# Kernel optimization log

Hardware: AMD Instinct MI355X
Metric: run time of the kernel (lower is better)

Reference implementation:

```python
import jax, jax.numpy as jnp
import numpy as np

N_TOKEN = 267735
D_PROJ = 1024
CUTOFF_ENDS = [0, 20000, 40000, 200000, 267735]
D_EMBS = [1024, 256, 64, 16]  # d_embed // div_val**i, div_val=4
EMB_SCALE = float(D_PROJ) ** 0.5


def setup_inputs() -> dict:
    key = jax.random.key(0)
    ks = jax.random.split(key, 9)
    inp = jax.random.randint(ks[0], (8, 2048), 0, N_TOKEN)
    d = {"inp": inp}
    for i in range(4):
        size = CUTOFF_ENDS[i + 1] - CUTOFF_ENDS[i]
        de = D_EMBS[i]
        d[f"emb{i}"] = jax.random.normal(ks[1 + 2 * i], (size, de), jnp.float32) * 0.02
        d[f"proj{i}"] = jax.random.normal(ks[2 + 2 * i], (D_PROJ, de), jnp.float32) * 0.02
    return d


def reference(inp, emb0, emb1, emb2, emb3, proj0, proj1, proj2, proj3):
    embs = [emb0, emb1, emb2, emb3]
    projs = [proj0, proj1, proj2, proj3]
    flat = inp.reshape(-1)  # [T]
    out = jnp.zeros((flat.shape[0], D_PROJ), jnp.float32)
    for i in range(4):
        l, r = CUTOFF_ENDS[i], CUTOFF_ENDS[i + 1]
        mask = (flat >= l) & (flat < r)  # clusters are disjoint
        idx = jnp.clip(flat - l, 0, r - l - 1)  # in-range dummy where masked out
        # gather [T, d_emb_i] then project to [T, d_proj] (F.linear with weight [d_proj, d_emb_i])
        e = jnp.einsum('td,pd->tp', embs[i][idx], projs[i])
        out = jnp.where(mask[:, None], e, out)
    return (out * EMB_SCALE).reshape(*inp.shape, D_PROJ)
```

## Files before the change

### kernel.cpp

```cpp
#include <hip/hip_runtime.h>


#define CUT0 20000
#define CUT1 40000
#define CUT2 200000

#define PB1 (1024 * 1024)
#define PB2 (PB1 + 1024 * 256)
#define PB3 (PB2 + 1024 * 64)
#define PBEND (PB3 + 1024 * 32)

typedef __attribute__((ext_vector_type(8))) short bf16x8;
typedef __attribute__((ext_vector_type(8))) unsigned short u16x8;
typedef __attribute__((ext_vector_type(4))) float f32x4;

__device__ __forceinline__ unsigned short f2bf(float f) {
    unsigned u = __float_as_uint(f);
    u += 0x7FFFu + ((u >> 16) & 1u);
    return (unsigned short)(u >> 16);
}

__device__ __forceinline__ u16x8 cvt8(const float* __restrict__ s) {
    float4 a = *(const float4*)s;
    float4 b = *(const float4*)(s + 4);
    return (u16x8){f2bf(a.x), f2bf(a.y), f2bf(a.z), f2bf(a.w),
                   f2bf(b.x), f2bf(b.y), f2bf(b.z), f2bf(b.w)};
}

__device__ __forceinline__ void gl_lds16(const unsigned short* g, unsigned short* s) {
    __builtin_amdgcn_global_load_lds(
        (const __attribute__((address_space(1))) void*)g,
        (__attribute__((address_space(3))) void*)s, 16, 0, 0);
}

__global__ __launch_bounds__(256)
void classify_convert(const int* __restrict__ inp, unsigned* __restrict__ counters,
                      unsigned* __restrict__ lists, int T,
                      const float* __restrict__ proj0, const float* __restrict__ proj1,
                      const float* __restrict__ proj2, const float* __restrict__ proj3,
                      unsigned short* __restrict__ projbf) {
    int t = blockIdx.x * 256 + threadIdx.x;
    int lane = threadIdx.x & 63;
    bool valid = (t < T);
    int id = valid ? inp[t] : 0;
    int c = -1, l = 0;
    if (valid) {
        if (id < CUT0)      { c = 0; l = 0; }
        else if (id < CUT1) { c = 1; l = CUT0; }
        else if (id < CUT2) { c = 2; l = CUT1; }
        else                { c = 3; l = CUT2; }
    }
    #pragma unroll
    for (int i = 0; i < 4; ++i) {
        unsigned long long m = __ballot(c == i);
        if (c == i) {
            int leader = __ffsll(m) - 1;
            unsigned base = 0;
            if (lane == leader) base = atomicAdd(&counters[i], (unsigned)__popcll(m));
            base = __shfl(base, leader);
            unsigned rank = (unsigned)__popcll(m & ((1ull << lane) - 1ull));
            lists[(size_t)i * T + base + rank] = ((unsigned)t << 18) | (unsigned)(id - l);
        }
    }
    const int stride = gridDim.x * 256;
    for (int u = t; u < PBEND / 8; u += stride) {
        int base = u * 8;
        u16x8 o;
        if (base < PB1)       o = cvt8(proj0 + base);
        else if (base < PB2)  o = cvt8(proj1 + (base - PB1));
        else if (base < PB3)  o = cvt8(proj2 + (base - PB2));
        else {
            int rel = base - PB3;
            int row = rel >> 5, col = rel & 31;
            if (col < 16) o = cvt8(proj3 + row * 16 + col);
            else          o = (u16x8){0, 0, 0, 0, 0, 0, 0, 0};
        }
        *(u16x8*)(projbf + base) = o;
    }
}

__global__ __launch_bounds__(256)
void gather_bf16(const float* __restrict__ emb0, const float* __restrict__ emb1,
                 const unsigned* __restrict__ lists, const unsigned* __restrict__ counters,
                 int T, unsigned short* __restrict__ ecomp) {
    const int c0 = (int)counters[0], c1 = (int)counters[1];
    const size_t off1 = (size_t)((c0 + 63) & ~63) * 1024;
    const int n0 = c0 << 7, n1 = c1 << 5;
    const int total = n0 + n1;
    const int stride = gridDim.x * 256;
    for (int u = blockIdx.x * 256 + threadIdx.x; u < total; u += stride) {
        int v = u;
        if (v < n0) {
            int r = v >> 7, j = v & 127;
            unsigned id = lists[r] & 0x3FFFFu;
            *(u16x8*)(ecomp + (size_t)r * 1024 + j * 8) = cvt8(emb0 + (size_t)id * 1024 + j * 8);
        } else {
            v -= n0;
            int r = v >> 5, j = v & 31;
            unsigned id = lists[T + r] & 0x3FFFFu;
            *(u16x8*)(ecomp + off1 + (size_t)r * 256 + j * 8) = cvt8(emb1 + (size_t)id * 256 + j * 8);
        }
    }
}

template<int EK, int PK>
__device__ __forceinline__
void tile_shallow(const float* __restrict__ Ef, const unsigned short* __restrict__ P,
                  const unsigned* __restrict__ list, int count, int mtile, int ntile,
                  float* __restrict__ out) {
    constexpr int KST = PK / 32;
    const int m0 = mtile * 64;
    const int rows = min(64, count - m0);
    const int py = ntile * 128;
    const int tid = (int)threadIdx.x;
    const int lane = tid & 63;
    const int w  = tid >> 6;
    const int ln = lane & 15;
    const int qd = lane >> 4;

    const int arow = w * 16 + ln;
    const unsigned aid = (arow < rows) ? (list[m0 + arow] & 0x3FFFFu) : 0u;
    const float* ea = Ef + (size_t)aid * EK;
    const unsigned short* pb = P + (size_t)(py + ln) * PK + qd * 8;

    f32x4 acc[8];
    #pragma unroll
    for (int ct = 0; ct < 8; ++ct) acc[ct] = (f32x4){0.f, 0.f, 0.f, 0.f};

    #pragma unroll
    for (int s = 0; s < KST; ++s) {
        const int k = s * 32 + qd * 8;
        u16x8 av;
        if (k + 8 <= EK) av = cvt8(ea + k);
        else             av = (u16x8){0, 0, 0, 0, 0, 0, 0, 0};
        bf16x8 a = *(const bf16x8*)&av;
        #pragma unroll
        for (int ct = 0; ct < 8; ++ct) {
            bf16x8 b = *(const bf16x8*)(pb + (size_t)ct * 16 * PK + s * 32);
            acc[ct] = __builtin_amdgcn_mfma_f32_16x16x32_bf16(a, b, acc[ct], 0, 0, 0);
        }
    }

    int trow[4];
    #pragma unroll
    for (int r = 0; r < 4; ++r) {
        int row = w * 16 + qd * 4 + r;
        trow[r] = (row < rows) ? (int)(list[m0 + row] >> 18) : -1;
    }
    #pragma unroll
    for (int ct = 0; ct < 8; ++ct)
        #pragma unroll
        for (int r = 0; r < 4; ++r)
            if (trow[r] >= 0)
                out[(size_t)trow[r] * 1024 + py + ct * 16 + ln] = acc[ct][r] * 32.0f;
}

__global__ __launch_bounds__(256)
void gemm_shallow(const float* __restrict__ emb2, const float* __restrict__ emb3,
                  const unsigned short* __restrict__ projbf,
                  const unsigned* __restrict__ lists, const unsigned* __restrict__ counters,
                  int T, float* __restrict__ out) {
    const int c2 = (int)counters[2], c3 = (int)counters[3];
    const int g2 = (c2 + 63) >> 6;
    const int gt = g2 + ((c3 + 63) >> 6);

    const int xcd = blockIdx.x & 7;
    const int slot = blockIdx.x >> 3;
    const int nslots = gridDim.x >> 3;

    for (int i = slot; ; i += nslots) {
        const int g = ((i >> 3) << 3) + xcd;
        if (g >= gt) break;
        const int nt = i & 7;
        if (g < g2) tile_shallow<64, 64>(emb2, projbf + PB2, lists + 2 * T, c2, g,      nt, out);
        else        tile_shallow<16, 32>(emb3, projbf + PB3, lists + 3 * T, c3, g - g2, nt, out);
    }
}

template<int KP>
__device__ __forceinline__
void tile_gemm_lds(const unsigned short* __restrict__ E, const unsigned short* __restrict__ P,
                   const unsigned* __restrict__ list, int count, int mtile, int ntile,
                   float* __restrict__ out,
                   unsigned short* E_s, unsigned short* P_s, unsigned* pk_s) {
    constexpr int NCH = KP / 64;
    const int m0 = mtile * 64;
    const int rows = min(64, count - m0);
    const int py = ntile * 128;
    const int tid = (int)threadIdx.x;
    const int lane = tid & 63;
    const int w  = tid >> 6;
    const int ln = lane & 15;
    const int qd = lane >> 4;

    if (tid < 64) pk_s[tid] = (tid < rows) ? list[m0 + tid] : 0u;

    const unsigned short* eb = E + (size_t)m0 * KP;
    const unsigned short* pg = P + (size_t)py * KP;

    auto STAGE = [&](int h, int ch) {
        const int k0 = ch * 64;
        #pragma unroll
        for (int it = 0; it < 2; ++it) {
            int i16 = it * 256 + tid;
            int row = i16 >> 3, cc = (i16 & 7) ^ (row & 7);
            gl_lds16(eb + (size_t)row * KP + k0 + cc * 8, E_s + h * (64 * 64) + i16 * 8);
        }
        #pragma unroll
        for (int it = 0; it < 4; ++it) {
            int i16 = it * 256 + tid;
            int row = i16 >> 3, cc = (i16 & 7) ^ (row & 7);
            gl_lds16(pg + (size_t)row * KP + k0 + cc * 8, P_s + h * (128 * 64) + i16 * 8);
        }
    };

    f32x4 acc[8];
    #pragma unroll
    for (int ct = 0; ct < 8; ++ct) acc[ct] = (f32x4){0.f, 0.f, 0.f, 0.f};

    STAGE(0, 0);
    __syncthreads();
    int cur = 0;
    for (int ch = 0; ch < NCH; ++ch) {
        if (ch + 1 < NCH) STAGE(cur ^ 1, ch + 1);
        const unsigned short* Eb = E_s + cur * (64 * 64);
        const unsigned short* Pb = P_s + cur * (128 * 64);
        const int ar = w * 16 + ln;
        #pragma unroll
        for (int s = 0; s < 2; ++s) {
            bf16x8 a = *(const bf16x8*)(Eb + ar * 64 + (((s * 4 + qd) ^ (ar & 7)) * 8));
            #pragma unroll
            for (int ct = 0; ct < 8; ++ct) {
                const int br = ct * 16 + ln;
                bf16x8 b = *(const bf16x8*)(Pb + br * 64 + (((s * 4 + qd) ^ (br & 7)) * 8));
                acc[ct] = __builtin_amdgcn_mfma_f32_16x16x32_bf16(a, b, acc[ct], 0, 0, 0);
            }
        }
        __syncthreads();
        cur ^= 1;
    }

    #pragma unroll
    for (int ct = 0; ct < 8; ++ct) {
        #pragma unroll
        for (int r = 0; r < 4; ++r) {
            int row = w * 16 + qd * 4 + r;
            if (row < rows) {
                int t = (int)(pk_s[row] >> 18);
                out[(size_t)t * 1024 + py + ct * 16 + ln] = acc[ct][r] * 32.0f;
            }
        }
    }
    __syncthreads();
}

__global__ __launch_bounds__(256)
void gemm_deep(const unsigned short* __restrict__ ecomp, const unsigned short* __restrict__ projbf,
               const unsigned* __restrict__ lists, const unsigned* __restrict__ counters,
               int T, float* __restrict__ out) {
    __shared__ unsigned short E_s[2 * 64 * 64];
    __shared__ unsigned short P_s[2 * 128 * 64];
    __shared__ unsigned pk_s[64];

    const int c0 = (int)counters[0], c1 = (int)counters[1];
    const size_t off1 = (size_t)((c0 + 63) & ~63) * 1024;
    const int g0 = (c0 + 63) >> 6;
    const int gt = g0 + ((c1 + 63) >> 6);

    const int xcd = blockIdx.x & 7;
    const int slot = blockIdx.x >> 3;
    const int nslots = gridDim.x >> 3;

    for (int i = slot; ; i += nslots) {
        const int g = ((i >> 3) << 3) + xcd;
        if (g >= gt) break;
        const int nt = i & 7;
        if (g < g0) tile_gemm_lds<1024>(ecomp,        projbf,       lists,     c0, g,      nt, out, E_s, P_s, pk_s);
        else        tile_gemm_lds< 256>(ecomp + off1, projbf + PB1, lists + T, c1, g - g0, nt, out, E_s, P_s, pk_s);
    }
}

extern "C" void kernel_launch(void* const* d_in, const int* in_sizes, int n_in,
                              void* d_out, int out_size, void* d_ws, size_t ws_size,
                              hipStream_t stream) {
    const int*   inp   = (const int*)d_in[0];
    const float* emb0  = (const float*)d_in[1];
    const float* proj0 = (const float*)d_in[2];
    const float* emb1  = (const float*)d_in[3];
    const float* proj1 = (const float*)d_in[4];
    const float* emb2  = (const float*)d_in[5];
    const float* proj2 = (const float*)d_in[6];
    const float* emb3  = (const float*)d_in[7];
    const float* proj3 = (const float*)d_in[8];
    float* out = (float*)d_out;
    const int T = in_sizes[0];

    unsigned* counters = (unsigned*)d_ws;
    unsigned* lists    = (unsigned*)((char*)d_ws + 256);
    size_t lists_b = ((size_t)4 * T * 4 + 255) & ~(size_t)255;
    unsigned short* projbf = (unsigned short*)((char*)d_ws + 256 + lists_b);
    unsigned short* ecomp  = projbf + PBEND;

    hipMemsetAsync(counters, 0, 16, stream);
    classify_convert<<<dim3(512), 256, 0, stream>>>(inp, counters, lists, T,
                                                    proj0, proj1, proj2, proj3, projbf);
    gather_bf16<<<dim3(768), 256, 0, stream>>>(emb0, emb1, lists, counters, T, ecomp);
    gemm_shallow<<<dim3(2048), 256, 0, stream>>>(emb2, emb3, projbf, lists, counters, T, out);
    gemm_deep<<<dim3(768), 256, 0, stream>>>(ecomp, projbf, lists, counters, T, out);
}
```

Measured before the change: 226.2 us.

## Fuse embedding gather into deep GEMM and merge all cluster GEMMs into one kernel

Removes the separate gather_bf16 pass: deep tiles now read fp32 embedding rows directly by token id, convert to bf16 in registers, and write them into swizzled LDS. The shallow and deep GEMM kernels are merged into a single persistent launch covering all four clusters. The LDS double buffer becomes a single buffer, cutting shared memory and allowing an occupancy hint of 4 blocks per CU. This avoids the bf16 staging round-trip through global memory and two launches. In exchange, each of the 8 N-tiles per row tile re-gathers and re-converts the fp32 embeddings, and loads are no longer overlapped with MFMA.

New measurement: 222.1 us. No clear change (-1.8%).

```diff
diff --git a/kernel.cpp b/kernel.cpp
--- a/kernel.cpp
+++ b/kernel.cpp
@@ -79,29 +79,6 @@
     }
 }
 
-__global__ __launch_bounds__(256)
-void gather_bf16(const float* __restrict__ emb0, const float* __restrict__ emb1,
-                 const unsigned* __restrict__ lists, const unsigned* __restrict__ counters,
-                 int T, unsigned short* __restrict__ ecomp) {
-    const int c0 = (int)counters[0], c1 = (int)counters[1];
-    const size_t off1 = (size_t)((c0 + 63) & ~63) * 1024;
-    const int n0 = c0 << 7, n1 = c1 << 5;
-    const int total = n0 + n1;
-    const int stride = gridDim.x * 256;
-    for (int u = blockIdx.x * 256 + threadIdx.x; u < total; u += stride) {
-        int v = u;
-        if (v < n0) {
-            int r = v >> 7, j = v & 127;
-            unsigned id = lists[r] & 0x3FFFFu;
-            *(u16x8*)(ecomp + (size_t)r * 1024 + j * 8) = cvt8(emb0 + (size_t)id * 1024 + j * 8);
-        } else {
-            v -= n0;
-            int r = v >> 5, j = v & 31;
-            unsigned id = lists[T + r] & 0x3FFFFu;
-            *(u16x8*)(ecomp + off1 + (size_t)r * 256 + j * 8) = cvt8(emb1 + (size_t)id * 256 + j * 8);
-        }
-    }
-}
 
 template<int EK, int PK>
 __device__ __forceinline__
@@ -155,35 +132,13 @@
                 out[(size_t)trow[r] * 1024 + py + ct * 16 + ln] = acc[ct][r] * 32.0f;
 }
 
-__global__ __launch_bounds__(256)
-void gemm_shallow(const float* __restrict__ emb2, const float* __restrict__ emb3,
-                  const unsigned short* __restrict__ projbf,
-                  const unsigned* __restrict__ lists, const unsigned* __restrict__ counters,
-                  int T, float* __restrict__ out) {
-    const int c2 = (int)counters[2], c3 = (int)counters[3];
-    const int g2 = (c2 + 63) >> 6;
-    const int gt = g2 + ((c3 + 63) >> 6);
-
-    const int xcd = blockIdx.x & 7;
-    const int slot = blockIdx.x >> 3;
-    const int nslots = gridDim.x >> 3;
-
-    for (int i = slot; ; i += nslots) {
-        const int g = ((i >> 3) << 3) + xcd;
-        if (g >= gt) break;
-        const int nt = i & 7;
-        if (g < g2) tile_shallow<64, 64>(emb2, projbf + PB2, lists + 2 * T, c2, g,      nt, out);
-        else        tile_shallow<16, 32>(emb3, projbf + PB3, lists + 3 * T, c3, g - g2, nt, out);
-    }
-}
-
-template<int KP>
+template<int EK>
 __device__ __forceinline__
-void tile_gemm_lds(const unsigned short* __restrict__ E, const unsigned short* __restrict__ P,
-                   const unsigned* __restrict__ list, int count, int mtile, int ntile,
-                   float* __restrict__ out,
-                   unsigned short* E_s, unsigned short* P_s, unsigned* pk_s) {
-    constexpr int NCH = KP / 64;
+void tile_deep(const float* __restrict__ Ef, const unsigned short* __restrict__ P,
+               const unsigned* __restrict__ list, int count, int mtile, int ntile,
+               float* __restrict__ out,
+               unsigned short* E_s, unsigned short* P_s, unsigned* pk_s) {
+    constexpr int NCH = EK / 64;
     const int m0 = mtile * 64;
     const int rows = min(64, count - m0);
     const int py = ntile * 128;
@@ -195,49 +150,45 @@
 
     if (tid < 64) pk_s[tid] = (tid < rows) ? list[m0 + tid] : 0u;
 
-    const unsigned short* eb = E + (size_t)m0 * KP;
-    const unsigned short* pg = P + (size_t)py * KP;
-
-    auto STAGE = [&](int h, int ch) {
+    const int srow = tid >> 2;
+    const int sq4  = tid & 3;
+    const unsigned sid = (srow < rows) ? (list[m0 + srow] & 0x3FFFFu) : 0u;
+    const float* erow = Ef + (size_t)sid * EK + sq4 * 16;
+    const unsigned short* pg = P + (size_t)py * EK;
+
+    f32x4 acc[8];
+    #pragma unroll
+    for (int ct = 0; ct < 8; ++ct) acc[ct] = (f32x4){0.f, 0.f, 0.f, 0.f};
+
+    for (int ch = 0; ch < NCH; ++ch) {
         const int k0 = ch * 64;
-        #pragma unroll
-        for (int it = 0; it < 2; ++it) {
-            int i16 = it * 256 + tid;
-            int row = i16 >> 3, cc = (i16 & 7) ^ (row & 7);
-            gl_lds16(eb + (size_t)row * KP + k0 + cc * 8, E_s + h * (64 * 64) + i16 * 8);
+        {
+            u16x8 h0 = cvt8(erow + k0);
+            u16x8 h1 = cvt8(erow + k0 + 8);
+            const int ci = sq4 * 2;
+            *(u16x8*)&E_s[srow * 64 + ((ci       ^ (srow & 7)) * 8)] = h0;
+            *(u16x8*)&E_s[srow * 64 + (((ci + 1) ^ (srow & 7)) * 8)] = h1;
         }
         #pragma unroll
         for (int it = 0; it < 4; ++it) {
             int i16 = it * 256 + tid;
             int row = i16 >> 3, cc = (i16 & 7) ^ (row & 7);
-            gl_lds16(pg + (size_t)row * KP + k0 + cc * 8, P_s + h * (128 * 64) + i16 * 8);
-        }
-    };
-
-    f32x4 acc[8];
-    #pragma unroll
-    for (int ct = 0; ct < 8; ++ct) acc[ct] = (f32x4){0.f, 0.f, 0.f, 0.f};
-
-    STAGE(0, 0);
-    __syncthreads();
-    int cur = 0;
-    for (int ch = 0; ch < NCH; ++ch) {
-        if (ch + 1 < NCH) STAGE(cur ^ 1, ch + 1);
-        const unsigned short* Eb = E_s + cur * (64 * 64);
-        const unsigned short* Pb = P_s + cur * (128 * 64);
+            gl_lds16(pg + (size_t)row * EK + k0 + cc * 8, P_s + i16 * 8);
+        }
+        __syncthreads();
+
         const int ar = w * 16 + ln;
         #pragma unroll
         for (int s = 0; s < 2; ++s) {
-            bf16x8 a = *(const bf16x8*)(Eb + ar * 64 + (((s * 4 + qd) ^ (ar & 7)) * 8));
+            bf16x8 a = *(const bf16x8*)(E_s + ar * 64 + (((s * 4 + qd) ^ (ar & 7)) * 8));
             #pragma unroll
             for (int ct = 0; ct < 8; ++ct) {
                 const int br = ct * 16 + ln;
-                bf16x8 b = *(const bf16x8*)(Pb + br * 64 + (((s * 4 + qd) ^ (br & 7)) * 8));
+                bf16x8 b = *(const bf16x8*)(P_s + br * 64 + (((s * 4 + qd) ^ (br & 7)) * 8));
                 acc[ct] = __builtin_amdgcn_mfma_f32_16x16x32_bf16(a, b, acc[ct], 0, 0, 0);
             }
         }
         __syncthreads();
-        cur ^= 1;
     }
 
     #pragma unroll
@@ -254,18 +205,22 @@
     __syncthreads();
 }
 
-__global__ __launch_bounds__(256)
-void gemm_deep(const unsigned short* __restrict__ ecomp, const unsigned short* __restrict__ projbf,
-               const unsigned* __restrict__ lists, const unsigned* __restrict__ counters,
-               int T, float* __restrict__ out) {
-    __shared__ unsigned short E_s[2 * 64 * 64];
-    __shared__ unsigned short P_s[2 * 128 * 64];
+__global__ __launch_bounds__(256, 4)
+void gemm_merged(const float* __restrict__ emb0, const float* __restrict__ emb1,
+                 const float* __restrict__ emb2, const float* __restrict__ emb3,
+                 const unsigned short* __restrict__ projbf,
+                 const unsigned* __restrict__ lists, const unsigned* __restrict__ counters,
+                 int T, float* __restrict__ out) {
+    __shared__ unsigned short E_s[64 * 64];
+    __shared__ unsigned short P_s[128 * 64];
     __shared__ unsigned pk_s[64];
 
     const int c0 = (int)counters[0], c1 = (int)counters[1];
-    const size_t off1 = (size_t)((c0 + 63) & ~63) * 1024;
+    const int c2 = (int)counters[2], c3 = (int)counters[3];
     const int g0 = (c0 + 63) >> 6;
-    const int gt = g0 + ((c1 + 63) >> 6);
+    const int g1 = g0 + ((c1 + 63) >> 6);
+    const int g2 = g1 + ((c2 + 63) >> 6);
+    const int g3 = g2 + ((c3 + 63) >> 6);
 
     const int xcd = blockIdx.x & 7;
     const int slot = blockIdx.x >> 3;
@@ -273,10 +228,12 @@
 
     for (int i = slot; ; i += nslots) {
         const int g = ((i >> 3) << 3) + xcd;
-        if (g >= gt) break;
+        if (g >= g3) break;
         const int nt = i & 7;
-        if (g < g0) tile_gemm_lds<1024>(ecomp,        projbf,       lists,     c0, g,      nt, out, E_s, P_s, pk_s);
-        else        tile_gemm_lds< 256>(ecomp + off1, projbf + PB1, lists + T, c1, g - g0, nt, out, E_s, P_s, pk_s);
+        if (g < g0)      tile_deep<1024>(emb0, projbf,       lists,         c0, g,      nt, out, E_s, P_s, pk_s);
+        else if (g < g1) tile_deep< 256>(emb1, projbf + PB1, lists + T,     c1, g - g0, nt, out, E_s, P_s, pk_s);
+        else if (g < g2) tile_shallow<64, 64>(emb2, projbf + PB2, lists + 2 * T, c2, g - g1, nt, out);
+        else             tile_shallow<16, 32>(emb3, projbf + PB3, lists + 3 * T, c3, g - g2, nt, out);
     }
 }
 
@@ -299,12 +256,10 @@
     unsigned* lists    = (unsigned*)((char*)d_ws + 256);
     size_t lists_b = ((size_t)4 * T * 4 + 255) & ~(size_t)255;
     unsigned short* projbf = (unsigned short*)((char*)d_ws + 256 + lists_b);
-    unsigned short* ecomp  = projbf + PBEND;
 
     hipMemsetAsync(counters, 0, 16, stream);
     classify_convert<<<dim3(512), 256, 0, stream>>>(inp, counters, lists, T,
                                                     proj0, proj1, proj2, proj3, projbf);
-    gather_bf16<<<dim3(768), 256, 0, stream>>>(emb0, emb1, lists, counters, T, ecomp);
-    gemm_shallow<<<dim3(2048), 256, 0, stream>>>(emb2, emb3, projbf, lists, counters, T, out);
-    gemm_deep<<<dim3(768), 256, 0, stream>>>(ecomp, projbf, lists, counters, T, out);
-}
+    gemm_merged<<<dim3(1024), 256, 0, stream>>>(emb0, emb1, emb2, emb3,
+                                                projbf, lists, counters, T, out);
+}
```

## Merge deep and shallow GEMM kernels into one single-buffered persistent launch

Applied to the files above, without the earlier changes.

Combines the gemm_shallow and gemm_deep launches into a single gemm_merged kernel that walks one tile space covering all four clusters. The deep tiles drop LDS double buffering, which halves shared memory per block so more blocks fit per CU (launch bounds now ask for 6), but global-to-LDS loads no longer overlap with MFMA work. The grid becomes 1536 blocks, which removes one kernel launch and the tail gap between the two GEMM phases. The risk is exposed load latency on the 1024-deep cluster-0 tiles, plus higher register pressure from the combined code paths.

Measured after the change: 234.3 us. 3.6% more time.

```diff
diff --git a/kernel.cpp b/kernel.cpp
--- a/kernel.cpp
+++ b/kernel.cpp
@@ -103,6 +103,7 @@
     }
 }
 
+
 template<int EK, int PK>
 __device__ __forceinline__
 void tile_shallow(const float* __restrict__ Ef, const unsigned short* __restrict__ P,
@@ -155,34 +156,12 @@
                 out[(size_t)trow[r] * 1024 + py + ct * 16 + ln] = acc[ct][r] * 32.0f;
 }
 
-__global__ __launch_bounds__(256)
-void gemm_shallow(const float* __restrict__ emb2, const float* __restrict__ emb3,
-                  const unsigned short* __restrict__ projbf,
-                  const unsigned* __restrict__ lists, const unsigned* __restrict__ counters,
-                  int T, float* __restrict__ out) {
-    const int c2 = (int)counters[2], c3 = (int)counters[3];
-    const int g2 = (c2 + 63) >> 6;
-    const int gt = g2 + ((c3 + 63) >> 6);
-
-    const int xcd = blockIdx.x & 7;
-    const int slot = blockIdx.x >> 3;
-    const int nslots = gridDim.x >> 3;
-
-    for (int i = slot; ; i += nslots) {
-        const int g = ((i >> 3) << 3) + xcd;
-        if (g >= gt) break;
-        const int nt = i & 7;
-        if (g < g2) tile_shallow<64, 64>(emb2, projbf + PB2, lists + 2 * T, c2, g,      nt, out);
-        else        tile_shallow<16, 32>(emb3, projbf + PB3, lists + 3 * T, c3, g - g2, nt, out);
-    }
-}
-
 template<int KP>
 __device__ __forceinline__
-void tile_gemm_lds(const unsigned short* __restrict__ E, const unsigned short* __restrict__ P,
-                   const unsigned* __restrict__ list, int count, int mtile, int ntile,
-                   float* __restrict__ out,
-                   unsigned short* E_s, unsigned short* P_s, unsigned* pk_s) {
+void tile_deep(const unsigned short* __restrict__ E, const unsigned short* __restrict__ P,
+               const unsigned* __restrict__ list, int count, int mtile, int ntile,
+               float* __restrict__ out,
+               unsigned short* E_s, unsigned short* P_s, unsigned* pk_s) {
     constexpr int NCH = KP / 64;
     const int m0 = mtile * 64;
     const int rows = min(64, count - m0);
@@ -198,46 +177,38 @@
     const unsigned short* eb = E + (size_t)m0 * KP;
     const unsigned short* pg = P + (size_t)py * KP;
 
-    auto STAGE = [&](int h, int ch) {
+    f32x4 acc[8];
+    #pragma unroll
+    for (int ct = 0; ct < 8; ++ct) acc[ct] = (f32x4){0.f, 0.f, 0.f, 0.f};
+
+    for (int ch = 0; ch < NCH; ++ch) {
         const int k0 = ch * 64;
         #pragma unroll
         for (int it = 0; it < 2; ++it) {
             int i16 = it * 256 + tid;
             int row = i16 >> 3, cc = (i16 & 7) ^ (row & 7);
-            gl_lds16(eb + (size_t)row * KP + k0 + cc * 8, E_s + h * (64 * 64) + i16 * 8);
+            gl_lds16(eb + (size_t)row * KP + k0 + cc * 8, E_s + i16 * 8);
         }
         #pragma unroll
         for (int it = 0; it < 4; ++it) {
             int i16 = it * 256 + tid;
             int row = i16 >> 3, cc = (i16 & 7) ^ (row & 7);
-            gl_lds16(pg + (size_t)row * KP + k0 + cc * 8, P_s + h * (128 * 64) + i16 * 8);
-        }
-    };
-
-    f32x4 acc[8];
-    #pragma unroll
-    for (int ct = 0; ct < 8; ++ct) acc[ct] = (f32x4){0.f, 0.f, 0.f, 0.f};
-
-    STAGE(0, 0);
-    __syncthreads();
-    int cur = 0;
-    for (int ch = 0; ch < NCH; ++ch) {
-        if (ch + 1 < NCH) STAGE(cur ^ 1, ch + 1);
-        const unsigned short* Eb = E_s + cur * (64 * 64);
-        const unsigned short* Pb = P_s + cur * (128 * 64);
+            gl_lds16(pg + (size_t)row * KP + k0 + cc * 8, P_s + i16 * 8);
+        }
+        __syncthreads();
+
         const int ar = w * 16 + ln;
         #pragma unroll
         for (int s = 0; s < 2; ++s) {
-            bf16x8 a = *(const bf16x8*)(Eb + ar * 64 + (((s * 4 + qd) ^ (ar & 7)) * 8));
+            bf16x8 a = *(const bf16x8*)(E_s + ar * 64 + (((s * 4 + qd) ^ (ar & 7)) * 8));
             #pragma unroll
             for (int ct = 0; ct < 8; ++ct) {
                 const int br = ct * 16 + ln;
-                bf16x8 b = *(const bf16x8*)(Pb + br * 64 + (((s * 4 + qd) ^ (br & 7)) * 8));
+                bf16x8 b = *(const bf16x8*)(P_s + br * 64 + (((s * 4 + qd) ^ (br & 7)) * 8));
                 acc[ct] = __builtin_amdgcn_mfma_f32_16x16x32_bf16(a, b, acc[ct], 0, 0, 0);
             }
         }
         __syncthreads();
-        cur ^= 1;
     }
 
     #pragma unroll
@@ -254,18 +225,23 @@
     __syncthreads();
 }
 
-__global__ __launch_bounds__(256)
-void gemm_deep(const unsigned short* __restrict__ ecomp, const unsigned short* __restrict__ projbf,
-               const unsigned* __restrict__ lists, const unsigned* __restrict__ counters,
-               int T, float* __restrict__ out) {
-    __shared__ unsigned short E_s[2 * 64 * 64];
-    __shared__ unsigned short P_s[2 * 128 * 64];
+__global__ __launch_bounds__(256, 6)
+void gemm_merged(const unsigned short* __restrict__ ecomp,
+                 const float* __restrict__ emb2, const float* __restrict__ emb3,
+                 const unsigned short* __restrict__ projbf,
+                 const unsigned* __restrict__ lists, const unsigned* __restrict__ counters,
+                 int T, float* __restrict__ out) {
+    __shared__ unsigned short E_s[64 * 64];
+    __shared__ unsigned short P_s[128 * 64];
     __shared__ unsigned pk_s[64];
 
     const int c0 = (int)counters[0], c1 = (int)counters[1];
+    const int c2 = (int)counters[2], c3 = (int)counters[3];
     const size_t off1 = (size_t)((c0 + 63) & ~63) * 1024;
     const int g0 = (c0 + 63) >> 6;
-    const int gt = g0 + ((c1 + 63) >> 6);
+    const int g1 = g0 + ((c1 + 63) >> 6);
+    const int g2 = g1 + ((c2 + 63) >> 6);
+    const int g3 = g2 + ((c3 + 63) >> 6);
 
     const int xcd = blockIdx.x & 7;
     const int slot = blockIdx.x >> 3;
@@ -273,10 +249,12 @@
 
     for (int i = slot; ; i += nslots) {
         const int g = ((i >> 3) << 3) + xcd;
-        if (g >= gt) break;
+        if (g >= g3) break;
         const int nt = i & 7;
-        if (g < g0) tile_gemm_lds<1024>(ecomp,        projbf,       lists,     c0, g,      nt, out, E_s, P_s, pk_s);
-        else        tile_gemm_lds< 256>(ecomp + off1, projbf + PB1, lists + T, c1, g - g0, nt, out, E_s, P_s, pk_s);
+        if (g < g0)      tile_deep<1024>(ecomp,        projbf,       lists,     c0, g,      nt, out, E_s, P_s, pk_s);
+        else if (g < g1) tile_deep< 256>(ecomp + off1, projbf + PB1, lists + T, c1, g - g0, nt, out, E_s, P_s, pk_s);
+        else if (g < g2) tile_shallow<64, 64>(emb2, projbf + PB2, lists + 2 * T, c2, g - g1, nt, out);
+        else             tile_shallow<16, 32>(emb3, projbf + PB3, lists + 3 * T, c3, g - g2, nt, out);
     }
 }
 
@@ -305,6 +283,6 @@
     classify_convert<<<dim3(512), 256, 0, stream>>>(inp, counters, lists, T,
                                                     proj0, proj1, proj2, proj3, projbf);
     gather_bf16<<<dim3(768), 256, 0, stream>>>(emb0, emb1, lists, counters, T, ecomp);
-    gemm_shallow<<<dim3(2048), 256, 0, stream>>>(emb2, emb3, projbf, lists, counters, T, out);
-    gemm_deep<<<dim3(768), 256, 0, stream>>>(ecomp, projbf, lists, counters, T, out);
-}
+    gemm_merged<<<dim3(1536), 256, 0, stream>>>(ecomp, emb2, emb3, projbf,
+                                                lists, counters, T, out);
+}
```
